# Performance work log

Measured on AMD Instinct MI355X. Metric: run time of the kernel, lower is better.

The kernel has to match this reference:

```python
import jax, jax.numpy as jnp
import numpy as np

BATCH, SEQ, IN_DIM, UNITS = 64, 512, 512, 1024

def _glorot(key, shape):
    fan_in, fan_out = shape
    lim = jnp.sqrt(6.0 / (fan_in + fan_out))
    return jax.random.uniform(key, shape, jnp.float32, -lim, lim)

def setup_inputs() -> dict:
    key = jax.random.key(0)
    ks = jax.random.split(key, 6)
    x = jax.random.normal(ks[0], (BATCH, SEQ, IN_DIM), dtype=jnp.float32)
    d = IN_DIM + UNITS
    W_f = _glorot(ks[1], (d, UNITS))
    W_i = _glorot(ks[2], (d, UNITS))
    W_o = _glorot(ks[3], (d, UNITS))
    W_c = _glorot(ks[4], (d, UNITS))
    b_f = jnp.ones((UNITS,), jnp.float32)  # unit_forget_bias=True
    b_i = jnp.zeros((UNITS,), jnp.float32)
    b_o = jnp.zeros((UNITS,), jnp.float32)
    b_c = jnp.zeros((UNITS,), jnp.float32)
    return {"x": x, "W_f": W_f, "W_i": W_i, "W_o": W_o, "W_c": W_c,
            "b_f": b_f, "b_i": b_i, "b_o": b_o, "b_c": b_c}

def reference(x, W_f, W_i, W_o, W_c, b_f, b_i, b_o, b_c):
    B = x.shape[0]
    h0 = jnp.zeros((B, UNITS), x.dtype)
    c0 = jnp.zeros((B, UNITS), x.dtype)

    def step(carry, x_t):
        h, c = carry
        xh = jnp.concatenate([x_t, h], axis=1)  # [B, IN_DIM+UNITS]
        f = jax.nn.sigmoid(xh @ W_f + b_f)
        i = jax.nn.sigmoid(xh @ W_i + b_i)
        c_cand = jnp.tanh(xh @ W_c + b_c)
        c_new = f * c + i * c_cand
        o = jax.nn.sigmoid(xh @ W_o + b_o)
        h_new = o * jnp.tanh(c_new)
        return (h_new, c_new), h_new

    x_tbf = jnp.swapaxes(x, 0, 1)  # [SEQ, B, IN_DIM]
    _, hs = jax.lax.scan(step, (h0, c0), x_tbf)
    return jnp.swapaxes(hs, 0, 1)  # [B, SEQ, UNITS]
```

## Files before the change

### kernel.cpp

```cpp
#include <hip/hip_runtime.h>
#include <hip/hip_bf16.h>

typedef __attribute__((ext_vector_type(8))) _Float16 half8;
typedef __attribute__((ext_vector_type(4))) _Float16 half4v;
typedef __attribute__((ext_vector_type(4))) float f32x4;
typedef __attribute__((ext_vector_type(2))) float f32x2;
typedef unsigned long long u64;

#define T_SEQ 512
#define N_B   64
#define D_IN  512
#define N_U   1024

#define OFF_CNT   0ull
#define OFF_HSEQ  65536ull
#define OFF_XB    (OFF_HSEQ + 513ull*131072ull)
#define OFF_WBT   (OFF_XB + 33554432ull)
#define OFF_WHT   (OFF_WBT + 4194304ull)
#define OFF_BIAS  (OFF_WHT + 8388608ull)

__device__ __forceinline__ float sigf(float x) { return 1.f / (1.f + __expf(-x)); }
__device__ __forceinline__ float tanhfast(float x) { return 2.f / (1.f + __expf(-2.f * x)) - 1.f; }

__global__ __launch_bounds__(256) void pack_x(const float* __restrict__ x, _Float16* __restrict__ xb) {
  size_t i4 = ((size_t)blockIdx.x * 256 + threadIdx.x) * 4;
  int m = (int)(i4 >> 9), k = (int)(i4 & 511);
  int t = m >> 6, b = m & 63;
  const float4 v = *(const float4*)(x + ((size_t)b * T_SEQ + t) * D_IN + k);
  half4v o; o.x = (_Float16)v.x; o.y = (_Float16)v.y; o.z = (_Float16)v.z; o.w = (_Float16)v.w;
  *(half4v*)(xb + i4) = o;
}

__global__ __launch_bounds__(256) void pack_w(const float* __restrict__ Wf, const float* __restrict__ Wi,
                                              const float* __restrict__ Wo, const float* __restrict__ Wc,
                                              _Float16* __restrict__ WbT, _Float16* __restrict__ WhT) {
  size_t i4 = ((size_t)blockIdx.x * 256 + threadIdx.x) * 4;
  int n = (int)(i4 / 1536), k = (int)(i4 % 1536);
  int g = n & 3, u = n >> 2;
  const float* W = (g == 0) ? Wf : (g == 1) ? Wi : (g == 2) ? Wo : Wc;
  half4v o;
  o.x = (_Float16)W[(size_t)(k + 0) * N_U + u];
  o.y = (_Float16)W[(size_t)(k + 1) * N_U + u];
  o.z = (_Float16)W[(size_t)(k + 2) * N_U + u];
  o.w = (_Float16)W[(size_t)(k + 3) * N_U + u];
  if (k < D_IN) *(half4v*)(WbT + (size_t)n * D_IN + k) = o;
  else          *(half4v*)(WhT + (size_t)n * N_U + (k - D_IN)) = o;
}

__global__ __launch_bounds__(256) void pack_b(const float* __restrict__ bf_, const float* __restrict__ bi_,
                                              const float* __restrict__ bo_, const float* __restrict__ bc_,
                                              float* __restrict__ biasv) {
  int n = blockIdx.x * 256 + threadIdx.x;
  int g = n & 3, u = n >> 2;
  biasv[n] = (g == 0) ? bf_[u] : (g == 1) ? bi_[u] : (g == 2) ? bo_[u] : bc_[u];
}

__global__ __launch_bounds__(256, 1) void lstm_rec(
    const _Float16* __restrict__ xb, const _Float16* __restrict__ WbT,
    const _Float16* __restrict__ WhT, const float* __restrict__ biasv,
    _Float16* __restrict__ hseq, float* __restrict__ out, unsigned* __restrict__ bar) {
  const int wg = blockIdx.x;
  const int tid = threadIdx.x;
  const int l = tid & 63, w = tid >> 6;
  const int col0 = wg * 32;
  const int lr = l & 15, lkb = (l >> 4) * 8;
  const int arow = w * 16 + lr;

  __shared__ half8 wlds[96 * 64];
  __shared__ float glds[64 * 36];

  for (int idx = tid; idx < 96 * 64; idx += 256) {
    int s = idx >> 6, l2 = idx & 63;
    int kk = s >> 1, nf = s & 1;
    int lr2 = l2 & 15, lkb2 = (l2 >> 4) * 8;
    int col = col0 + nf * 16 + lr2;
    const _Float16* src = (kk < 16)
      ? WbT + (size_t)col * D_IN + kk * 32 + lkb2
      : WhT + (size_t)col * N_U + (kk - 16) * 32 + lkb2;
    wlds[idx] = *(const half8*)src;
  }

  const int eb  = tid >> 2;
  const int eu2 = (tid & 3) * 2;
  const int ug  = wg * 8 + eu2;
  float c0 = 0.f, c1 = 0.f;
  const float bv0 = biasv[col0 + lr];
  const float bv1 = biasv[col0 + 16 + lr];

  unsigned* flags = bar;

  __syncthreads();

  for (int g = 0; g < T_SEQ; g++) {
    const _Float16* xa = xb + ((size_t)g * N_B + arow) * D_IN + lkb;
    half8 xf[16];
#pragma unroll
    for (int j = 0; j < 16; j++) xf[j] = *(const half8*)(xa + j * 32);

    f32x4 a0 = {bv0, bv0, bv0, bv0};
    f32x4 a1 = {bv1, bv1, bv1, bv1};
    f32x4 b0 = {0.f, 0.f, 0.f, 0.f};
    f32x4 b1 = {0.f, 0.f, 0.f, 0.f};
#pragma unroll
    for (int j = 0; j < 8; j++) {
      a0 = __builtin_amdgcn_mfma_f32_16x16x32_f16(xf[j], wlds[(j * 2 + 0) * 64 + l], a0, 0, 0, 0);
      a1 = __builtin_amdgcn_mfma_f32_16x16x32_f16(xf[j], wlds[(j * 2 + 1) * 64 + l], a1, 0, 0, 0);
      b0 = __builtin_amdgcn_mfma_f32_16x16x32_f16(xf[j + 8], wlds[((j + 8) * 2 + 0) * 64 + l], b0, 0, 0, 0);
      b1 = __builtin_amdgcn_mfma_f32_16x16x32_f16(xf[j + 8], wlds[((j + 8) * 2 + 1) * 64 + l], b1, 0, 0, 0);
    }

    if (g > 0) {
      if (tid < 128) {
        while (__hip_atomic_load(&flags[tid], __ATOMIC_RELAXED, __HIP_MEMORY_SCOPE_AGENT) < (unsigned)g)
          __builtin_amdgcn_s_sleep(1);
      }
      asm volatile("" ::: "memory");
      __syncthreads();
    }

    const _Float16* hp = hseq + (size_t)g * (N_B * N_U) + (size_t)arow * N_U + lkb;
    half8 hf[32];
#pragma unroll
    for (int j = 0; j < 32; j++) hf[j] = *(const half8*)(hp + j * 32);
#pragma unroll
    for (int j = 0; j < 16; j++) {
      a0 = __builtin_amdgcn_mfma_f32_16x16x32_f16(hf[j], wlds[((16 + j) * 2 + 0) * 64 + l], a0, 0, 0, 0);
      a1 = __builtin_amdgcn_mfma_f32_16x16x32_f16(hf[j], wlds[((16 + j) * 2 + 1) * 64 + l], a1, 0, 0, 0);
      b0 = __builtin_amdgcn_mfma_f32_16x16x32_f16(hf[j + 16], wlds[((32 + j) * 2 + 0) * 64 + l], b0, 0, 0, 0);
      b1 = __builtin_amdgcn_mfma_f32_16x16x32_f16(hf[j + 16], wlds[((32 + j) * 2 + 1) * 64 + l], b1, 0, 0, 0);
    }
    a0 += b0;
    a1 += b1;

#pragma unroll
    for (int r = 0; r < 4; r++) {
      int row = w * 16 + (l >> 4) * 4 + r;
      glds[row * 36 + lr] = a0[r];
      glds[row * 36 + 16 + lr] = a1[r];
    }
    __syncthreads();

    const float* grow = &glds[eb * 36 + eu2 * 4];
    float F0 = grow[0], I0 = grow[1], O0 = grow[2], G0 = grow[3];
    float F1 = grow[4], I1 = grow[5], O1 = grow[6], G1 = grow[7];
    c0 = sigf(F0) * c0 + sigf(I0) * tanhfast(G0);
    c1 = sigf(F1) * c1 + sigf(I1) * tanhfast(G1);
    float h0v = sigf(O0) * tanhfast(c0);
    float h1v = sigf(O1) * tanhfast(c1);

    unsigned hw;
    { union { _Float16 h[2]; unsigned u; } pk; pk.h[0] = (_Float16)h0v; pk.h[1] = (_Float16)h1v; hw = pk.u; }
    unsigned* hn = (unsigned*)(hseq + (size_t)(g + 1) * (N_B * N_U) + (size_t)eb * N_U + ug);
    __hip_atomic_store(hn, hw, __ATOMIC_RELAXED, __HIP_MEMORY_SCOPE_AGENT);

    __syncthreads();
    if (tid == 0)
      __hip_atomic_store(&flags[wg], (unsigned)(g + 1), __ATOMIC_RELAXED, __HIP_MEMORY_SCOPE_AGENT);

    f32x2 ov; ov.x = h0v; ov.y = h1v;
    __builtin_nontemporal_store(ov, (f32x2*)(out + ((size_t)eb * T_SEQ + g) * N_U + ug));
  }
}

extern "C" void kernel_launch(void* const* d_in, const int* in_sizes, int n_in,
                              void* d_out, int out_size, void* d_ws, size_t ws_size,
                              hipStream_t stream) {
  const float* x  = (const float*)d_in[0];
  const float* Wf = (const float*)d_in[1];
  const float* Wi = (const float*)d_in[2];
  const float* Wo = (const float*)d_in[3];
  const float* Wc = (const float*)d_in[4];
  const float* bf_ = (const float*)d_in[5];
  const float* bi_ = (const float*)d_in[6];
  const float* bo_ = (const float*)d_in[7];
  const float* bc_ = (const float*)d_in[8];
  float* out = (float*)d_out;

  char* ws = (char*)d_ws;
  unsigned* bar = (unsigned*)(ws + OFF_CNT);
  _Float16* hseq = (_Float16*)(ws + OFF_HSEQ);
  _Float16* xb   = (_Float16*)(ws + OFF_XB);
  _Float16* WbT  = (_Float16*)(ws + OFF_WBT);
  _Float16* WhT  = (_Float16*)(ws + OFF_WHT);
  float* biasv = (float*)(ws + OFF_BIAS);

  hipMemsetAsync(d_ws, 0, 1 << 20, stream);
  pack_x<<<16384, 256, 0, stream>>>(x, xb);
  pack_w<<<6144, 256, 0, stream>>>(Wf, Wi, Wo, Wc, WbT, WhT);
  pack_b<<<16, 256, 0, stream>>>(bf_, bi_, bo_, bc_, biasv);

  lstm_rec<<<128, 256, 0, stream>>>(xb, WbT, WhT, biasv, hseq, out, bar);
}
```

Before: 3.565 ms.

## Pipeline next-step input GEMM, replace LDS gate exchange with swizzles, per-wave barrier

Reorders each workgroup's weight columns so the four gates of a unit sit in adjacent lanes. Gates are then gathered with ds_swizzle quad transposes instead of an LDS round-trip plus __syncthreads. The x-projection for step g+1 is now computed after h is published, overlapping it with other workgroups' progress. The block-wide barrier is replaced by per-wave polling of all 128 flags and an LDS atomic counter that lets the last wave raise the global flag. This cuts sync latency on the serial critical path, at the cost of more complex memory-ordering assumptions and every wave polling global flags.

```diff
diff --git a/kernel.cpp b/kernel.cpp
--- a/kernel.cpp
+++ b/kernel.cpp
@@ -55,6 +55,26 @@
   biasv[n] = (g == 0) ? bf_[u] : (g == 1) ? bi_[u] : (g == 2) ? bo_[u] : bc_[u];
 }
 
+__device__ __forceinline__ void quadtr(f32x4 v, int gg, float& F, float& I, float& O, float& G) {
+  const bool o1 = gg & 1, o2 = gg & 2;
+  float s01 = o1 ? v[0] : v[1];
+  float s23 = o1 ? v[2] : v[3];
+  float r01 = __int_as_float(__builtin_amdgcn_ds_swizzle(__float_as_int(s01), 0x041F));
+  float r23 = __int_as_float(__builtin_amdgcn_ds_swizzle(__float_as_int(s23), 0x041F));
+  float x0 = o1 ? r01 : v[0];
+  float x1 = o1 ? v[1] : r01;
+  float x2 = o1 ? r23 : v[2];
+  float x3 = o1 ? v[3] : r23;
+  float s02 = o2 ? x0 : x2;
+  float s13 = o2 ? x1 : x3;
+  float r02 = __int_as_float(__builtin_amdgcn_ds_swizzle(__float_as_int(s02), 0x081F));
+  float r13 = __int_as_float(__builtin_amdgcn_ds_swizzle(__float_as_int(s13), 0x081F));
+  F = o2 ? r02 : x0;
+  I = o2 ? r13 : x1;
+  O = o2 ? x2 : r02;
+  G = o2 ? x3 : r13;
+}
+
 __global__ __launch_bounds__(256, 1) void lstm_rec(
     const _Float16* __restrict__ xb, const _Float16* __restrict__ WbT,
     const _Float16* __restrict__ WhT, const float* __restrict__ biasv,
@@ -62,87 +82,84 @@
   const int wg = blockIdx.x;
   const int tid = threadIdx.x;
   const int l = tid & 63, w = tid >> 6;
-  const int col0 = wg * 32;
   const int lr = l & 15, lkb = (l >> 4) * 8;
   const int arow = w * 16 + lr;
+  const int uu = lr >> 2, gg = l & 3;
+  const int u0 = wg * 8 + 2 * uu;
+  const int R  = w * 16 + (l >> 4) * 4 + gg;
 
   __shared__ half8 wlds[96 * 64];
-  __shared__ float glds[64 * 36];
-
+  __shared__ unsigned lds_cnt;
+
+  if (tid == 0) lds_cnt = 0u;
   for (int idx = tid; idx < 96 * 64; idx += 256) {
     int s = idx >> 6, l2 = idx & 63;
     int kk = s >> 1, nf = s & 1;
-    int lr2 = l2 & 15, lkb2 = (l2 >> 4) * 8;
-    int col = col0 + nf * 16 + lr2;
+    int uu2 = (l2 & 15) >> 2, gg2 = l2 & 3, lkb2 = (l2 >> 4) * 8;
+    int col = (wg * 8 + 2 * uu2 + nf) * 4 + gg2;
     const _Float16* src = (kk < 16)
       ? WbT + (size_t)col * D_IN + kk * 32 + lkb2
       : WhT + (size_t)col * N_U + (kk - 16) * 32 + lkb2;
     wlds[idx] = *(const half8*)src;
   }
 
-  const int eb  = tid >> 2;
-  const int eu2 = (tid & 3) * 2;
-  const int ug  = wg * 8 + eu2;
+  const float bv0 = biasv[(size_t)u0 * 4 + gg];
+  const float bv1 = biasv[(size_t)(u0 + 1) * 4 + gg];
   float c0 = 0.f, c1 = 0.f;
-  const float bv0 = biasv[col0 + lr];
-  const float bv1 = biasv[col0 + 16 + lr];
-
   unsigned* flags = bar;
 
   __syncthreads();
 
+  half8 xfn[16];
+  {
+    const _Float16* xa = xb + (size_t)arow * D_IN + lkb;
+#pragma unroll
+    for (int j = 0; j < 16; j++) xfn[j] = *(const half8*)(xa + j * 32);
+  }
+  f32x4 a0 = {bv0, bv0, bv0, bv0};
+  f32x4 a1 = {bv1, bv1, bv1, bv1};
+#pragma unroll
+  for (int j = 0; j < 16; j++) {
+    a0 = __builtin_amdgcn_mfma_f32_16x16x32_f16(xfn[j], wlds[(j * 2 + 0) * 64 + l], a0, 0, 0, 0);
+    a1 = __builtin_amdgcn_mfma_f32_16x16x32_f16(xfn[j], wlds[(j * 2 + 1) * 64 + l], a1, 0, 0, 0);
+  }
+
   for (int g = 0; g < T_SEQ; g++) {
-    const _Float16* xa = xb + ((size_t)g * N_B + arow) * D_IN + lkb;
-    half8 xf[16];
-#pragma unroll
-    for (int j = 0; j < 16; j++) xf[j] = *(const half8*)(xa + j * 32);
-
-    f32x4 a0 = {bv0, bv0, bv0, bv0};
-    f32x4 a1 = {bv1, bv1, bv1, bv1};
+    if (g > 0) {
+      bool ok;
+      do {
+        unsigned f0 = __hip_atomic_load(&flags[l],      __ATOMIC_RELAXED, __HIP_MEMORY_SCOPE_AGENT);
+        unsigned f1 = __hip_atomic_load(&flags[64 + l], __ATOMIC_RELAXED, __HIP_MEMORY_SCOPE_AGENT);
+        ok = (f0 >= (unsigned)g) && (f1 >= (unsigned)g);
+      } while (!__all(ok));
+      asm volatile("" ::: "memory");
+    }
+
+    const _Float16* hp = hseq + (size_t)g * (N_B * N_U) + (size_t)arow * N_U + lkb;
+    half8 hf[32];
+#pragma unroll
+    for (int j = 0; j < 32; j++) hf[j] = *(const half8*)(hp + j * 32);
+
+    const int gn = (g + 1 < T_SEQ) ? g + 1 : 0;
+    const _Float16* xa = xb + ((size_t)gn * N_B + arow) * D_IN + lkb;
+#pragma unroll
+    for (int j = 0; j < 16; j++) xfn[j] = *(const half8*)(xa + j * 32);
+
     f32x4 b0 = {0.f, 0.f, 0.f, 0.f};
     f32x4 b1 = {0.f, 0.f, 0.f, 0.f};
 #pragma unroll
-    for (int j = 0; j < 8; j++) {
-      a0 = __builtin_amdgcn_mfma_f32_16x16x32_f16(xf[j], wlds[(j * 2 + 0) * 64 + l], a0, 0, 0, 0);
-      a1 = __builtin_amdgcn_mfma_f32_16x16x32_f16(xf[j], wlds[(j * 2 + 1) * 64 + l], a1, 0, 0, 0);
-      b0 = __builtin_amdgcn_mfma_f32_16x16x32_f16(xf[j + 8], wlds[((j + 8) * 2 + 0) * 64 + l], b0, 0, 0, 0);
-      b1 = __builtin_amdgcn_mfma_f32_16x16x32_f16(xf[j + 8], wlds[((j + 8) * 2 + 1) * 64 + l], b1, 0, 0, 0);
-    }
-
-    if (g > 0) {
-      if (tid < 128) {
-        while (__hip_atomic_load(&flags[tid], __ATOMIC_RELAXED, __HIP_MEMORY_SCOPE_AGENT) < (unsigned)g)
-          __builtin_amdgcn_s_sleep(1);
-      }
-      asm volatile("" ::: "memory");
-      __syncthreads();
-    }
-
-    const _Float16* hp = hseq + (size_t)g * (N_B * N_U) + (size_t)arow * N_U + lkb;
-    half8 hf[32];
-#pragma unroll
-    for (int j = 0; j < 32; j++) hf[j] = *(const half8*)(hp + j * 32);
-#pragma unroll
     for (int j = 0; j < 16; j++) {
-      a0 = __builtin_amdgcn_mfma_f32_16x16x32_f16(hf[j], wlds[((16 + j) * 2 + 0) * 64 + l], a0, 0, 0, 0);
-      a1 = __builtin_amdgcn_mfma_f32_16x16x32_f16(hf[j], wlds[((16 + j) * 2 + 1) * 64 + l], a1, 0, 0, 0);
+      a0 = __builtin_amdgcn_mfma_f32_16x16x32_f16(hf[j],      wlds[((16 + j) * 2 + 0) * 64 + l], a0, 0, 0, 0);
+      a1 = __builtin_amdgcn_mfma_f32_16x16x32_f16(hf[j],      wlds[((16 + j) * 2 + 1) * 64 + l], a1, 0, 0, 0);
       b0 = __builtin_amdgcn_mfma_f32_16x16x32_f16(hf[j + 16], wlds[((32 + j) * 2 + 0) * 64 + l], b0, 0, 0, 0);
       b1 = __builtin_amdgcn_mfma_f32_16x16x32_f16(hf[j + 16], wlds[((32 + j) * 2 + 1) * 64 + l], b1, 0, 0, 0);
     }
     a0 += b0;
     a1 += b1;
 
-#pragma unroll
-    for (int r = 0; r < 4; r++) {
-      int row = w * 16 + (l >> 4) * 4 + r;
-      glds[row * 36 + lr] = a0[r];
-      glds[row * 36 + 16 + lr] = a1[r];
-    }
-    __syncthreads();
-
-    const float* grow = &glds[eb * 36 + eu2 * 4];
-    float F0 = grow[0], I0 = grow[1], O0 = grow[2], G0 = grow[3];
-    float F1 = grow[4], I1 = grow[5], O1 = grow[6], G1 = grow[7];
+    float F0, I0, O0, G0, F1, I1, O1, G1;
+    quadtr(a0, gg, F0, I0, O0, G0);
+    quadtr(a1, gg, F1, I1, O1, G1);
     c0 = sigf(F0) * c0 + sigf(I0) * tanhfast(G0);
     c1 = sigf(F1) * c1 + sigf(I1) * tanhfast(G1);
     float h0v = sigf(O0) * tanhfast(c0);
@@ -150,15 +167,32 @@
 
     unsigned hw;
     { union { _Float16 h[2]; unsigned u; } pk; pk.h[0] = (_Float16)h0v; pk.h[1] = (_Float16)h1v; hw = pk.u; }
-    unsigned* hn = (unsigned*)(hseq + (size_t)(g + 1) * (N_B * N_U) + (size_t)eb * N_U + ug);
+    unsigned* hn = (unsigned*)(hseq + (size_t)(g + 1) * (N_B * N_U) + (size_t)R * N_U + u0);
     __hip_atomic_store(hn, hw, __ATOMIC_RELAXED, __HIP_MEMORY_SCOPE_AGENT);
 
-    __syncthreads();
-    if (tid == 0)
-      __hip_atomic_store(&flags[wg], (unsigned)(g + 1), __ATOMIC_RELAXED, __HIP_MEMORY_SCOPE_AGENT);
+    a0 = f32x4{bv0, bv0, bv0, bv0};
+    a1 = f32x4{bv1, bv1, bv1, bv1};
+#pragma unroll
+    for (int j = 0; j < 8; j++) {
+      a0 = __builtin_amdgcn_mfma_f32_16x16x32_f16(xfn[j], wlds[(j * 2 + 0) * 64 + l], a0, 0, 0, 0);
+      a1 = __builtin_amdgcn_mfma_f32_16x16x32_f16(xfn[j], wlds[(j * 2 + 1) * 64 + l], a1, 0, 0, 0);
+    }
+
+    asm volatile("s_waitcnt vmcnt(0)" ::: "memory");
+    if (l == 0) {
+      unsigned old = atomicAdd(&lds_cnt, 1u);
+      if (old == 4u * (unsigned)g + 3u)
+        __hip_atomic_store(&flags[wg], (unsigned)(g + 1), __ATOMIC_RELAXED, __HIP_MEMORY_SCOPE_AGENT);
+    }
+
+#pragma unroll
+    for (int j = 8; j < 16; j++) {
+      a0 = __builtin_amdgcn_mfma_f32_16x16x32_f16(xfn[j], wlds[(j * 2 + 0) * 64 + l], a0, 0, 0, 0);
+      a1 = __builtin_amdgcn_mfma_f32_16x16x32_f16(xfn[j], wlds[(j * 2 + 1) * 64 + l], a1, 0, 0, 0);
+    }
 
     f32x2 ov; ov.x = h0v; ov.y = h1v;
-    __builtin_nontemporal_store(ov, (f32x2*)(out + ((size_t)eb * T_SEQ + g) * N_U + ug));
+    __builtin_nontemporal_store(ov, (f32x2*)(out + ((size_t)R * T_SEQ + g) * N_U + u0));
   }
 }
 
```

New measurement: 4.542 ms. 1.27x slower.
